# Kernel optimization log

Hardware: AMD Instinct MI355X
Metric: run time of the kernel (lower is better)

## Reference

```python
import jax, jax.numpy as jnp
import numpy as np

B, S, E = 4, 2048, 768
H = 12
D = E // H  # 64

def setup_inputs() -> dict:
    key = jax.random.key(0)
    k_x, k_wqkv, k_wproj = jax.random.split(key, 3)
    x = jax.random.normal(k_x, (B, S, E), dtype=jnp.float32)
    w_qkv = jax.random.normal(k_wqkv, (E, 3 * E), dtype=jnp.float32) * 0.02
    b_qkv = jnp.zeros((3 * E,), dtype=jnp.float32)
    w_proj = jax.random.normal(k_wproj, (E, E), dtype=jnp.float32) * 0.02
    b_proj = jnp.zeros((E,), dtype=jnp.float32)
    return {"x": x, "w_qkv": w_qkv, "b_qkv": b_qkv, "w_proj": w_proj, "b_proj": b_proj}

def reference(x, w_qkv, b_qkv, w_proj, b_proj):
    # fused QKV projection: [B,S,E] -> [B,S,3E]
    qkv = jnp.einsum("bse,ef->bsf", x, w_qkv) + b_qkv
    qkv = qkv.reshape(B, S, 3, H, D)
    q, k, v = qkv[:, :, 0], qkv[:, :, 1], qkv[:, :, 2]  # [B,S,H,D]
    scale = 1.0 / jnp.sqrt(jnp.asarray(D, dtype=x.dtype))
    # causal scaled dot-product attention (explicit score matrix, as in module)
    scores = jnp.einsum("bshd,bthd->bhst", q, k) * scale  # [B,H,S,S]
    causal = jnp.tril(jnp.ones((S, S), dtype=bool))
    scores = jnp.where(causal, scores, jnp.finfo(scores.dtype).min)
    probs = jax.nn.softmax(scores, axis=-1)
    attn = jnp.einsum("bhst,bthd->bshd", probs, v).reshape(B, S, E)
    # output projection
    out = jnp.einsum("bse,ef->bsf", attn, w_proj) + b_proj
    return out
```

## Files before the change

kernel.cpp:

```cpp
#include <hip/hip_runtime.h>

#define SDIM 2048
#define EDIM 768
#define HDIM 12
#define DDIM 64
#define BDIM 4
#define MROWS (BDIM * SDIM)
#define NQKV (3 * EDIM)
#define NBH (BDIM * HDIM)
#define NTILE 32
#define NPAIR 16

typedef __attribute__((ext_vector_type(8))) short s16x8;
typedef __attribute__((ext_vector_type(4))) float f32x4;
typedef __attribute__((ext_vector_type(2))) unsigned int u32x2;

__device__ __forceinline__ short f2b(float x) {
  union { float f; unsigned u; } v; v.f = x;
  unsigned r = v.u + 0x7fffu + ((v.u >> 16) & 1u);
  return (short)(r >> 16);
}

__device__ __forceinline__ unsigned cvtpk(float lo, float hi) {
  unsigned r;
  asm volatile("v_cvt_pk_bf16_f32 %0, %1, %2" : "=v"(r) : "v"(lo), "v"(hi));
  return r;
}

__device__ __forceinline__ void gld16(const void* g, void* l) {
  __builtin_amdgcn_global_load_lds(
      (const __attribute__((address_space(1))) unsigned int*)g,
      (__attribute__((address_space(3))) unsigned int*)l, 16, 0, 0);
}

__global__ __launch_bounds__(256) void convert_bf16(
    const float* __restrict__ in, short* __restrict__ out, int n4) {
  int i = blockIdx.x * 256 + threadIdx.x;
  int stride = gridDim.x * 256;
  for (; i < n4; i += stride) {
    float4 v = ((const float4*)in)[i];
    short4 o;
    o.x = f2b(v.x); o.y = f2b(v.y); o.z = f2b(v.z); o.w = f2b(v.w);
    ((short4*)out)[i] = o;
  }
}

__global__ __launch_bounds__(256) void transpose_bf16(
    const float* __restrict__ in, short* __restrict__ out, int K, int N) {
  __shared__ float t[32][33];
  int n0 = blockIdx.x * 32, k0 = blockIdx.y * 32;
  int tx = threadIdx.x & 31, ty = threadIdx.x >> 5;
#pragma unroll
  for (int i = 0; i < 4; ++i)
    t[ty + 8 * i][tx] = in[(size_t)(k0 + ty + 8 * i) * N + n0 + tx];
  __syncthreads();
#pragma unroll
  for (int i = 0; i < 4; ++i)
    out[(size_t)(n0 + ty + 8 * i) * K + k0 + tx] = f2b(t[tx][ty + 8 * i]);
}

__global__ __launch_bounds__(256) void gemm_bf16(
    const short* __restrict__ A, const short* __restrict__ Bt,
    const float* __restrict__ bias, int M, int N, int K, int mode,
    short* __restrict__ qout, short* __restrict__ kout,
    short* __restrict__ vout, float* __restrict__ fout) {
  __shared__ char lds[2][16384];
  const int tid = threadIdx.x;
  const int l = tid & 63, w = tid >> 6;
  const int lr = l & 15, g = l >> 4;
  const int bm = blockIdx.y * 128, bn = blockIdx.x * 128;
  const int wm = w >> 1, wn = w & 1;

  const int srow = w * 32 + (l >> 2);
  const int sc8 = (((l & 3) ^ ((l >> 3) & 3)) << 3);
  const short* Ap0 = A + (size_t)(bm + srow) * K + sc8;
  const short* Bp0 = Bt + (size_t)(bn + srow) * K + sc8;

  f32x4 acc[4][4];
  const f32x4 z4 = {0.f, 0.f, 0.f, 0.f};
#pragma unroll
  for (int m = 0; m < 4; ++m)
#pragma unroll
    for (int n = 0; n < 4; ++n) acc[m][n] = z4;

  const int nt = K >> 5;
  {
    char* Ad = lds[0] + w * 2048;
    gld16(Ap0, Ad);
    gld16(Ap0 + 16 * K, Ad + 1024);
    gld16(Bp0, Ad + 8192);
    gld16(Bp0 + 16 * K, Ad + 9216);
  }
  __syncthreads();

  const int swz = ((lr >> 1) & 3) << 4;
  int buf = 0;
  for (int t = 0; t < nt; ++t) {
    if (t + 1 < nt) {
      char* Ad = lds[buf ^ 1] + w * 2048;
      const short* Ap = Ap0 + (t + 1) * 32;
      const short* Bp = Bp0 + (t + 1) * 32;
      gld16(Ap, Ad);
      gld16(Ap + 16 * K, Ad + 1024);
      gld16(Bp, Ad + 8192);
      gld16(Bp + 16 * K, Ad + 9216);
    }
    const char* Ab = lds[buf];
    const char* Bb = lds[buf] + 8192;
    s16x8 af[4], bfr[4];
#pragma unroll
    for (int m = 0; m < 4; ++m)
      af[m] = *(const s16x8*)(Ab + (wm * 64 + m * 16 + lr) * 64 + ((g << 4) ^ swz));
#pragma unroll
    for (int n = 0; n < 4; ++n)
      bfr[n] = *(const s16x8*)(Bb + (wn * 64 + n * 16 + lr) * 64 + ((g << 4) ^ swz));
#pragma unroll
    for (int m = 0; m < 4; ++m)
#pragma unroll
      for (int n = 0; n < 4; ++n)
        acc[m][n] = __builtin_amdgcn_mfma_f32_16x16x32_bf16(af[m], bfr[n],
                                                            acc[m][n], 0, 0, 0);
    __syncthreads();
    buf ^= 1;
  }

#pragma unroll
  for (int m = 0; m < 4; ++m) {
    int rbase = bm + wm * 64 + m * 16 + g * 4;
#pragma unroll
    for (int n = 0; n < 4; ++n) {
      int col = bn + wn * 64 + n * 16 + lr;
      float bv = bias[col];
      if (mode == 0) {
        int which = (col >= 1536) ? 2 : (col >= 768 ? 1 : 0);
        int rem = col - which * 768;
        int h = rem >> 6, d = rem & 63;
#pragma unroll
        for (int i = 0; i < 4; ++i) {
          int r = rbase + i;
          int b = r >> 11, s = r & 2047;
          short o = f2b(acc[m][n][i] + bv);
          size_t bh = (size_t)b * HDIM + h;
          if (which == 0)      qout[(bh * SDIM + s) * DDIM + d] = o;
          else if (which == 1) kout[(bh * SDIM + s) * DDIM + d] = o;
          else                 vout[(bh * DDIM + d) * SDIM + s] = o;
        }
      } else {
#pragma unroll
        for (int i = 0; i < 4; ++i)
          fout[(size_t)(rbase + i) * N + col] = acc[m][n][i] + bv;
      }
    }
  }
}

__global__ __launch_bounds__(256) void attn_mfma3(
    const short* __restrict__ qb, const short* __restrict__ kb,
    const short* __restrict__ vb, short* __restrict__ ao) {
  __shared__ short kvbuf[2][8192];
  __shared__ short pstrip[4][1024];

  const int tid = threadIdx.x;
  const int l = tid & 63, w = tid >> 6;
  const int lr = l & 15, g = l >> 4;
  const int swz = (lr & 7) << 4;

  const int lin = blockIdx.x;
  const int xcd = lin & 7;
  const int idx = lin >> 3;
  const int bh = xcd * 6 + (idx >> 4);
  const int pair = idx & 15;
  const int tiles[2] = {NTILE - 1 - pair, pair};

  const int b = bh / HDIM, h = bh % HDIM;
  const size_t base = (size_t)bh * SDIM * DDIM;

  const int srow = w * 16 + (l >> 3);
  const int sc = (l & 7) ^ (srow & 7);
  const size_t koff0 = (size_t)srow * DDIM + sc * 8;
  const size_t koff1 = (size_t)(srow + 8) * DDIM + sc * 8;
  const size_t voff0 = (size_t)srow * SDIM + sc * 8;
  const size_t voff1 = (size_t)(srow + 8) * SDIM + sc * 8;

  const float SC = 0.125f * 1.4426950408889634f;
  char* sw = (char*)pstrip[w];

  for (int half = 0; half < 2; ++half) {
    const int tile = tiles[half];
    const int q0w = tile * 64 + w * 16;

    s16x8 qa[2];
#pragma unroll
    for (int s = 0; s < 2; ++s)
      qa[s] = *(const s16x8*)(qb + base + (size_t)(q0w + lr) * DDIM + s * 32 + g * 8);

    const f32x4 z4 = {0.f, 0.f, 0.f, 0.f};
    f32x4 acco[4];
#pragma unroll
    for (int nd = 0; nd < 4; ++nd) acco[nd] = z4;
    float mrun = -1e30f, lsum = 0.f;

    int cur = 0;
    {
      char* kd = (char*)kvbuf[cur] + w * 2048;
      const short* kp = kb + base;
      const short* vp = vb + base;
      gld16(kp + koff0, kd);
      gld16(kp + koff1, kd + 1024);
      gld16(vp + voff0, kd + 8192);
      gld16(vp + voff1, kd + 9216);
    }
    __syncthreads();

    for (int kt = 0; kt <= tile; ++kt) {
      if (kt < tile) {
        char* kd = (char*)kvbuf[cur ^ 1] + w * 2048;
        const short* kp = kb + base + (size_t)(kt + 1) * 64 * DDIM;
        const short* vp = vb + base + (size_t)(kt + 1) * 64;
        gld16(kp + koff0, kd);
        gld16(kp + koff1, kd + 1024);
        gld16(vp + voff0, kd + 8192);
        gld16(vp + voff1, kd + 9216);
      }

      const char* Kb = (const char*)kvbuf[cur];
      const char* Vb = Kb + 8192;

      f32x4 sacc[4];
#pragma unroll
      for (int nt = 0; nt < 4; ++nt) sacc[nt] = z4;
      __builtin_amdgcn_s_setprio(1);
#pragma unroll
      for (int s = 0; s < 2; ++s)
#pragma unroll
        for (int nt = 0; nt < 4; ++nt) {
          s16x8 kf = *(const s16x8*)(Kb + nt * 2048 + lr * 128 +
                                     ((s * 64 + g * 16) ^ swz));
          sacc[nt] = __builtin_amdgcn_mfma_f32_16x16x32_bf16(kf, qa[s],
                                                             sacc[nt], 0, 0, 0);
        }
      __builtin_amdgcn_s_setprio(0);

      if (kt == tile) {
        const int rloc = w * 16 + lr;
#pragma unroll
        for (int nt = 0; nt < 4; ++nt)
#pragma unroll
          for (int i = 0; i < 4; ++i)
            if (nt * 16 + g * 4 + i > rloc) sacc[nt][i] = -1e30f;
      }

      float pmax = -1e30f;
#pragma unroll
      for (int nt = 0; nt < 4; ++nt)
#pragma unroll
        for (int i = 0; i < 4; ++i) pmax = fmaxf(pmax, sacc[nt][i]);
      pmax = fmaxf(pmax, __shfl_xor(pmax, 16, 64));
      pmax = fmaxf(pmax, __shfl_xor(pmax, 32, 64));

      if (__any(pmax > mrun + 44.0f)) {
        float nm = fmaxf(mrun, pmax);
        float al = exp2f((mrun - nm) * SC);
        lsum *= al;
#pragma unroll
        for (int nd = 0; nd < 4; ++nd)
#pragma unroll
          for (int i = 0; i < 4; ++i) acco[nd][i] *= al;
        mrun = nm;
      }

      const float msc = mrun * SC;
#pragma unroll
      for (int nt = 0; nt < 4; ++nt) {
        float p0 = exp2f(__builtin_fmaf(sacc[nt][0], SC, -msc));
        float p1 = exp2f(__builtin_fmaf(sacc[nt][1], SC, -msc));
        float p2 = exp2f(__builtin_fmaf(sacc[nt][2], SC, -msc));
        float p3 = exp2f(__builtin_fmaf(sacc[nt][3], SC, -msc));
        lsum += (p0 + p1) + (p2 + p3);
        u32x2 pk = {cvtpk(p0, p1), cvtpk(p2, p3)};
        *(u32x2*)(sw + lr * 128 + (((nt * 32 + g * 8) ^ swz))) = pk;
      }

      __builtin_amdgcn_s_setprio(1);
#pragma unroll
      for (int s = 0; s < 2; ++s) {
        s16x8 pf = *(const s16x8*)(sw + lr * 128 + ((s * 64 + g * 16) ^ swz));
#pragma unroll
        for (int nd = 0; nd < 4; ++nd) {
          s16x8 vf = *(const s16x8*)(Vb + nd * 2048 + lr * 128 +
                                     ((s * 64 + g * 16) ^ swz));
          acco[nd] = __builtin_amdgcn_mfma_f32_16x16x32_bf16(vf, pf,
                                                             acco[nd], 0, 0, 0);
        }
      }
      __builtin_amdgcn_s_setprio(0);

      __syncthreads();
      cur ^= 1;
    }

    lsum += __shfl_xor(lsum, 16, 64);
    lsum += __shfl_xor(lsum, 32, 64);
    float inv = 1.0f / lsum;
    size_t orow = ((size_t)b * SDIM + q0w + lr) * EDIM + h * DDIM;
#pragma unroll
    for (int nd = 0; nd < 4; ++nd) {
      unsigned lo = cvtpk(acco[nd][0] * inv, acco[nd][1] * inv);
      unsigned hi = cvtpk(acco[nd][2] * inv, acco[nd][3] * inv);
      *(unsigned*)(ao + orow + nd * 16 + g * 4) = lo;
      *(unsigned*)(ao + orow + nd * 16 + g * 4 + 2) = hi;
    }
  }
}

extern "C" void kernel_launch(void* const* d_in, const int* in_sizes, int n_in,
                              void* d_out, int out_size, void* d_ws,
                              size_t ws_size, hipStream_t stream) {
  const float* x = (const float*)d_in[0];
  const float* w_qkv = (const float*)d_in[1];
  const float* b_qkv = (const float*)d_in[2];
  const float* w_proj = (const float*)d_in[3];
  const float* b_proj = (const float*)d_in[4];
  float* out = (float*)d_out;

  char* p = (char*)d_ws;
  short* xb = (short*)p;      p += (size_t)MROWS * EDIM * 2;
  short* wqkvt = (short*)p;   p += (size_t)NQKV * EDIM * 2;
  short* wprojt = (short*)p;  p += (size_t)EDIM * EDIM * 2;
  short* qbuf = (short*)p;    p += (size_t)NBH * SDIM * DDIM * 2;
  short* kbuf = (short*)p;    p += (size_t)NBH * SDIM * DDIM * 2;
  short* vbuf = (short*)p;    p += (size_t)NBH * SDIM * DDIM * 2;
  short* aob = (short*)p;     p += (size_t)MROWS * EDIM * 2;

  dim3 blk(256);
  convert_bf16<<<dim3(2048), blk, 0, stream>>>(x, xb, MROWS * EDIM / 4);
  transpose_bf16<<<dim3(NQKV / 32, EDIM / 32), blk, 0, stream>>>(w_qkv, wqkvt, EDIM, NQKV);
  transpose_bf16<<<dim3(EDIM / 32, EDIM / 32), blk, 0, stream>>>(w_proj, wprojt, EDIM, EDIM);
  gemm_bf16<<<dim3(NQKV / 128, MROWS / 128), blk, 0, stream>>>(
      xb, wqkvt, b_qkv, MROWS, NQKV, EDIM, 0, qbuf, kbuf, vbuf, nullptr);
  attn_mfma3<<<dim3(NPAIR * NBH), blk, 0, stream>>>(qbuf, kbuf, vbuf, aob);
  gemm_bf16<<<dim3(EDIM / 128, MROWS / 128), blk, 0, stream>>>(
      aob, wprojt, b_proj, MROWS, EDIM, EDIM, 1, nullptr, nullptr, nullptr, out);
}
```

Baseline: 165.2 us.

## Triple-buffer GEMM LDS staging and use raw v_exp_f32 in attention softmax

```diff
diff --git a/kernel.cpp b/kernel.cpp
--- a/kernel.cpp
+++ b/kernel.cpp
@@ -27,6 +27,12 @@
   return r;
 }
 
+__device__ __forceinline__ float fexp2(float x) {
+  float r;
+  asm("v_exp_f32 %0, %1" : "=v"(r) : "v"(x));
+  return r;
+}
+
 __device__ __forceinline__ void gld16(const void* g, void* l) {
   __builtin_amdgcn_global_load_lds(
       (const __attribute__((address_space(1))) unsigned int*)g,
@@ -64,7 +70,7 @@
     const float* __restrict__ bias, int M, int N, int K, int mode,
     short* __restrict__ qout, short* __restrict__ kout,
     short* __restrict__ vout, float* __restrict__ fout) {
-  __shared__ char lds[2][16384];
+  __shared__ char lds[3][16384];
   const int tid = threadIdx.x;
   const int l = tid & 63, w = tid >> 6;
   const int lr = l & 15, g = l >> 4;
@@ -83,30 +89,32 @@
 #pragma unroll
     for (int n = 0; n < 4; ++n) acc[m][n] = z4;
 
+#define STAGE(dst, t)                          \
+  {                                            \
+    char* Ad = (dst) + w * 2048;               \
+    const short* Ap = Ap0 + (t) * 32;          \
+    const short* Bp = Bp0 + (t) * 32;          \
+    gld16(Ap, Ad);                             \
+    gld16(Ap + 16 * K, Ad + 1024);             \
+    gld16(Bp, Ad + 8192);                      \
+    gld16(Bp + 16 * K, Ad + 9216);             \
+  }
+
   const int nt = K >> 5;
-  {
-    char* Ad = lds[0] + w * 2048;
-    gld16(Ap0, Ad);
-    gld16(Ap0 + 16 * K, Ad + 1024);
-    gld16(Bp0, Ad + 8192);
-    gld16(Bp0 + 16 * K, Ad + 9216);
-  }
-  __syncthreads();
+  STAGE(lds[0], 0);
+  STAGE(lds[1], 1);
+  asm volatile("s_waitcnt vmcnt(4)" ::: "memory");
+  __builtin_amdgcn_s_barrier();
 
   const int swz = ((lr >> 1) & 3) << 4;
-  int buf = 0;
+  int bc = 0;
   for (int t = 0; t < nt; ++t) {
-    if (t + 1 < nt) {
-      char* Ad = lds[buf ^ 1] + w * 2048;
-      const short* Ap = Ap0 + (t + 1) * 32;
-      const short* Bp = Bp0 + (t + 1) * 32;
-      gld16(Ap, Ad);
-      gld16(Ap + 16 * K, Ad + 1024);
-      gld16(Bp, Ad + 8192);
-      gld16(Bp + 16 * K, Ad + 9216);
-    }
-    const char* Ab = lds[buf];
-    const char* Bb = lds[buf] + 8192;
+    if (t + 2 < nt) {
+      int bs = bc + 2; if (bs >= 3) bs -= 3;
+      STAGE(lds[bs], t + 2);
+    }
+    const char* Ab = lds[bc];
+    const char* Bb = lds[bc] + 8192;
     s16x8 af[4], bfr[4];
 #pragma unroll
     for (int m = 0; m < 4; ++m)
@@ -120,9 +128,16 @@
       for (int n = 0; n < 4; ++n)
         acc[m][n] = __builtin_amdgcn_mfma_f32_16x16x32_bf16(af[m], bfr[n],
                                                             acc[m][n], 0, 0, 0);
-    __syncthreads();
-    buf ^= 1;
-  }
+    if (t + 2 < nt) {
+      asm volatile("s_waitcnt vmcnt(4)" ::: "memory");
+      __builtin_amdgcn_s_barrier();
+    } else if (t + 1 < nt) {
+      asm volatile("s_waitcnt vmcnt(0)" ::: "memory");
+      __builtin_amdgcn_s_barrier();
+    }
+    if (++bc == 3) bc = 0;
+  }
+#undef STAGE
 
 #pragma unroll
   for (int m = 0; m < 4; ++m) {
@@ -250,17 +265,17 @@
             if (nt * 16 + g * 4 + i > rloc) sacc[nt][i] = -1e30f;
       }
 
-      float pmax = -1e30f;
-#pragma unroll
-      for (int nt = 0; nt < 4; ++nt)
-#pragma unroll
-        for (int i = 0; i < 4; ++i) pmax = fmaxf(pmax, sacc[nt][i]);
+      float t0 = fmaxf(fmaxf(sacc[0][0], sacc[0][1]), fmaxf(sacc[0][2], sacc[0][3]));
+      float t1 = fmaxf(fmaxf(sacc[1][0], sacc[1][1]), fmaxf(sacc[1][2], sacc[1][3]));
+      float t2 = fmaxf(fmaxf(sacc[2][0], sacc[2][1]), fmaxf(sacc[2][2], sacc[2][3]));
+      float t3 = fmaxf(fmaxf(sacc[3][0], sacc[3][1]), fmaxf(sacc[3][2], sacc[3][3]));
+      float pmax = fmaxf(fmaxf(t0, t1), fmaxf(t2, t3));
       pmax = fmaxf(pmax, __shfl_xor(pmax, 16, 64));
       pmax = fmaxf(pmax, __shfl_xor(pmax, 32, 64));
 
       if (__any(pmax > mrun + 44.0f)) {
         float nm = fmaxf(mrun, pmax);
-        float al = exp2f((mrun - nm) * SC);
+        float al = fexp2((mrun - nm) * SC);
         lsum *= al;
 #pragma unroll
         for (int nd = 0; nd < 4; ++nd)
@@ -272,10 +287,10 @@
       const float msc = mrun * SC;
 #pragma unroll
       for (int nt = 0; nt < 4; ++nt) {
-        float p0 = exp2f(__builtin_fmaf(sacc[nt][0], SC, -msc));
-        float p1 = exp2f(__builtin_fmaf(sacc[nt][1], SC, -msc));
-        float p2 = exp2f(__builtin_fmaf(sacc[nt][2], SC, -msc));
-        float p3 = exp2f(__builtin_fmaf(sacc[nt][3], SC, -msc));
+        float p0 = fexp2(__builtin_fmaf(sacc[nt][0], SC, -msc));
+        float p1 = fexp2(__builtin_fmaf(sacc[nt][1], SC, -msc));
+        float p2 = fexp2(__builtin_fmaf(sacc[nt][2], SC, -msc));
+        float p3 = fexp2(__builtin_fmaf(sacc[nt][3], SC, -msc));
         lsum += (p0 + p1) + (p2 + p3);
         u32x2 pk = {cvtpk(p0, p1), cvtpk(p2, p3)};
         *(u32x2*)(sw + lr * 128 + (((nt * 32 + g * 8) ^ swz))) = pk;
```

Result: faster. 151.1 us (-8.5%).
